# Kernel optimization log

Measured on AMD Instinct MI355X. Metric: run time of the kernel, lower is better.

## Reference

```python
import jax, jax.numpy as jnp
import numpy as np

B, S, D = 4, 1024, 1024      # batch, seq, dim
H = 1024                     # moe_inter_dim
E = 16                       # n_routed_experts
K = 2                        # n_activated_experts (top-k)
N_IN = 2                     # experts that consume x instead of embeddings
NSH = 2                      # n_shared_experts


def setup_inputs() -> dict:
    key = jax.random.key(0)
    ks = jax.random.split(key, 10)
    s = 0.02
    return {
        "embeddings": jax.random.normal(ks[0], (B, S, D), dtype=jnp.float32),
        "x": jax.random.normal(ks[1], (B * S, D), dtype=jnp.float32),
        "gate_w": jax.random.normal(ks[2], (E, D), dtype=jnp.float32) * s,
        "W1": jax.random.normal(ks[3], (E, D, H), dtype=jnp.float32) * s,
        "B1": jnp.zeros((E, H), dtype=jnp.float32),
        "W2": jax.random.normal(ks[4], (E, H, D), dtype=jnp.float32) * s,
        "B2": jnp.zeros((E, D), dtype=jnp.float32),
        "W3": jax.random.normal(ks[5], (E, D, H), dtype=jnp.float32) * s,
        "B3": jnp.zeros((E, H), dtype=jnp.float32),
        "sW1": jax.random.normal(ks[6], (D, NSH * H), dtype=jnp.float32) * s,
        "sB1": jnp.zeros((NSH * H,), dtype=jnp.float32),
        "sW2": jax.random.normal(ks[7], (NSH * H, D), dtype=jnp.float32) * s,
        "sB2": jnp.zeros((D,), dtype=jnp.float32),
    }


def _experts(inp, W1, B1, W2, B2, W3, B3):
    # SwiGLU expert applied for a stack of experts: inp [T,D], W* [e,...]
    h = jax.nn.silu(jnp.einsum('td,edh->eth', inp, W1) + B1[:, None, :]) \
        * (jnp.einsum('td,edh->eth', inp, W3) + B3[:, None, :])
    return jnp.einsum('eth,ehd->etd', h, W2) + B2[:, None, :]


def reference(embeddings, x, gate_w, W1, B1, W2, B2, W3, B3, sW1, sB1, sW2, sB2):
    shape = embeddings.shape
    emb = embeddings.reshape(-1, D)                       # [T, D]
    # Gate: softmax scores in fp32; n_groups==1, bias is None -> no group masking
    scores = jax.nn.softmax((emb @ gate_w.T).astype(jnp.float32), axis=-1)  # [T, E]
    top_w, top_i = jax.lax.top_k(scores, K)               # weights == gathered original_scores
    weights = top_w.astype(emb.dtype)                     # route_scale = 1.0
    # Combine coefficient per (token, expert): sum of routing weights of slots hitting e
    c = jnp.einsum('tk,tke->te', weights,
                   jax.nn.one_hot(top_i, E, dtype=weights.dtype))  # [T, E]
    # First N_IN experts consume x; the rest consume the embeddings
    out_in = _experts(x, W1[:N_IN], B1[:N_IN], W2[:N_IN], B2[:N_IN], W3[:N_IN], B3[:N_IN])
    out_emb = _experts(emb, W1[N_IN:], B1[N_IN:], W2[N_IN:], B2[N_IN:], W3[N_IN:], B3[N_IN:])
    y = jnp.einsum('te,etd->td', c, jnp.concatenate([out_in, out_emb], axis=0))
    # Shared experts (applied to every token)
    z = jax.nn.silu(emb @ sW1 + sB1) @ sW2 + sB2
    return (y + z).reshape(shape)
```

## Files before the change

### kernel.cpp

```cpp
#include <hip/hip_runtime.h>

#define T_TOK 4096
#define DIM   1024
#define HID   1024
#define NEXP  16
#define HSH   2048
#define NIN   2
#define MT_MAX 80

typedef __attribute__((ext_vector_type(8))) short bf8_t;
typedef __attribute__((ext_vector_type(4))) float f4_t;

__device__ __forceinline__ ushort f2b(float f) {
  unsigned u = __float_as_uint(f);
  u = (u + 0x7FFFu + ((u >> 16) & 1u)) >> 16;
  return (ushort)u;
}

__device__ __forceinline__ int tp_off(int r, int c) {
  return r * 64 + ((((c >> 3) ^ (r & 7)) << 3) | (c & 7));
}
__device__ __forceinline__ size_t tp_idx(int row, int col, int KT) {
  return ((size_t)((row >> 7) * KT + (col >> 6)) << 13) + tp_off(row & 127, col & 63);
}

__device__ __forceinline__ void gl_lds16(const ushort* g, ushort* l) {
  __builtin_amdgcn_global_load_lds(
      (const __attribute__((address_space(1))) void*)g,
      (__attribute__((address_space(3))) void*)l, 16, 0, 0);
}

__device__ __forceinline__ int src_off(int sr, int rd, int cp, int h) {
  const int cg = h * 4 + (cp ^ ((rd >> 1) & 3));
  return sr * 64 + ((cg ^ (sr & 7)) << 3);
}

template<bool DUAL>
__device__ __forceinline__ void mfma_tp(
    const ushort* pA00, const ushort* pA01,
    const ushort* pA10, const ushort* pA11,
    const ushort* b1T, const ushort* b3T,
    int oB00, int oB01, int oB10, int oB11,
    int nkt, ushort* As, ushort* Bs1, ushort* Bs3,
    f4_t acc1[4][4], f4_t acc3[4][4], int tid)
{
  const int lane = tid & 63, w = tid >> 6;
  const int wm = w & 1, wn = w >> 1;
  const int quad = lane >> 4, lr = lane & 15;
  const int dst0 = w * 1024 + lane * 8;

  auto stage = [&](int koff, ushort* dA, ushort* dB1, ushort* dB3,
                   const ushort* a0, const ushort* a1, int ob0, int ob1) {
    gl_lds16(a0 + koff, dA + dst0);
    gl_lds16(a1 + koff, dA + dst0 + 512);
    gl_lds16(b1T + ob0 + koff, dB1 + dst0);
    gl_lds16(b1T + ob1 + koff, dB1 + dst0 + 512);
    if (DUAL) {
      gl_lds16(b3T + ob0 + koff, dB3 + dst0);
      gl_lds16(b3T + ob1 + koff, dB3 + dst0 + 512);
    }
  };
  auto compute = [&](const ushort* A, const ushort* B1, const ushort* B3) {
    bf8_t af[4];
    #pragma unroll
    for (int mi = 0; mi < 4; mi++) {
      const int r = wm * 64 + mi * 16 + lr;
      af[mi] = *(const bf8_t*)&A[r * 32 + ((quad ^ ((r >> 1) & 3)) << 3)];
    }
    #pragma unroll
    for (int ni = 0; ni < 4; ni++) {
      const int n = wn * 64 + ni * 16 + lr;
      const bf8_t b1 = *(const bf8_t*)&B1[n * 32 + ((quad ^ ((n >> 1) & 3)) << 3)];
      #pragma unroll
      for (int mi = 0; mi < 4; mi++)
        acc1[mi][ni] = __builtin_amdgcn_mfma_f32_16x16x32_bf16(af[mi], b1, acc1[mi][ni], 0, 0, 0);
      if (DUAL) {
        const bf8_t b3 = *(const bf8_t*)&B3[n * 32 + ((quad ^ ((n >> 1) & 3)) << 3)];
        #pragma unroll
        for (int mi = 0; mi < 4; mi++)
          acc3[mi][ni] = __builtin_amdgcn_mfma_f32_16x16x32_bf16(af[mi], b3, acc3[mi][ni], 0, 0, 0);
      }
    }
  };

  stage(0, As, Bs1, Bs3, pA00, pA10, oB00, oB10);
  __syncthreads();
  for (int kt = 0; kt < nkt; kt++) {
    const int ko = kt << 13;
    stage(ko, As + 4096, Bs1 + 4096, Bs3 + 4096, pA01, pA11, oB01, oB11);
    compute(As, Bs1, Bs3);
    __syncthreads();
    if (kt + 1 < nkt)
      stage(ko + 8192, As, Bs1, Bs3, pA00, pA10, oB00, oB10);
    compute(As + 4096, Bs1 + 4096, Bs3 + 4096);
    __syncthreads();
  }
}

__device__ __forceinline__ void tr_chunk(const float* __restrict__ src,
                                         ushort* __restrict__ dst,
                                         int R, int C, int band, int c, int tid,
                                         ushort* ts)
{
  const int KT = R >> 6;
  const int k0 = band * 64;
  #pragma unroll
  for (int i = 0; i < 16; i++) {
    const int idx = i * 256 + tid;
    const int r = idx >> 6, c4 = idx & 63;
    const float4 v = *(const float4*)(src + (size_t)(k0 + r) * C + c * 256 + c4 * 4);
    ushort4 u;
    u.x = f2b(v.x); u.y = f2b(v.y); u.z = f2b(v.z); u.w = f2b(v.w);
    *(ushort4*)&ts[r * 256 + ((c4 ^ ((r >> 3) & 7)) << 2)] = u;
  }
  __syncthreads();
  #pragma unroll
  for (int s = 0; s < 8; s++) {
    const int idx = s * 256 + tid;
    const int n = idx >> 3, kc = idx & 7;
    ushort o[8];
    #pragma unroll
    for (int j = 0; j < 8; j++)
      o[j] = ts[(kc * 8 + j) * 256 + (((n >> 2) ^ kc) << 2) + (n & 3)];
    *(uint4*)&dst[tp_idx(c * 256 + n, k0 + kc * 8, KT)] = *(uint4*)o;
  }
}

#define PREP_BLOCKS 4864
__launch_bounds__(256, 5)
__global__ void prep(const float* __restrict__ emb, const float* __restrict__ x_,
                     const float* __restrict__ gw,
                     const float* __restrict__ W1, const float* __restrict__ W3,
                     const float* __restrict__ W2,
                     const float* __restrict__ sW1, const float* __restrict__ sW2,
                     ushort* __restrict__ etp, ushort* __restrict__ xtp,
                     ushort* __restrict__ w1tp, ushort* __restrict__ w3tp,
                     ushort* __restrict__ w2tp,
                     ushort* __restrict__ sw1tp, ushort* __restrict__ sw2tp,
                     int* __restrict__ eA, int* __restrict__ eB,
                     float* __restrict__ wA, float* __restrict__ wB)
{
  __shared__ ushort ts[64 * 256];
  const int b = blockIdx.x;
  const int t = threadIdx.x;

  if (b < 3328) {
    const float* src; ushort* dst; int R, C, band, chunk;
    if (b < 3072) {
      const int z = b >> 6, rem = b & 63;
      band = rem >> 2; chunk = rem & 3;
      const int e = z & 15;
      src = ((z < 16) ? W1 : (z < 32) ? W3 : W2) + ((size_t)e << 20);
      dst = ((z < 16) ? w1tp : (z < 32) ? w3tp : w2tp) + ((size_t)e << 20);
      R = 1024; C = 1024;
    } else if (b < 3200) {
      const int i = b - 3072; band = i >> 3; chunk = i & 7;
      src = sW1; dst = sw1tp; R = 1024; C = 2048;
    } else {
      const int i = b - 3200; band = i >> 2; chunk = i & 3;
      src = sW2; dst = sw2tp; R = 2048; C = 1024;
    }
    tr_chunk(src, dst, R, C, band, chunk, t, ts);
  } else if (b < 4352) {
    const int w = t >> 6, lane = t & 63;
    const int tok = (b - 3328) * 4 + w;
    const float* er = emb + (size_t)tok * DIM + lane * 4;
    const float4 a0 = *(const float4*)(er);
    const float4 a1 = *(const float4*)(er + 256);
    const float4 a2 = *(const float4*)(er + 512);
    const float4 a3 = *(const float4*)(er + 768);
    float pe[NEXP];
    #pragma unroll
    for (int e = 0; e < NEXP; e++) {
      const float* gr = gw + (size_t)e * DIM + lane * 4;
      const float4 g0 = *(const float4*)(gr);
      const float4 g1 = *(const float4*)(gr + 256);
      const float4 g2 = *(const float4*)(gr + 512);
      const float4 g3 = *(const float4*)(gr + 768);
      float p = a0.x * g0.x + a0.y * g0.y + a0.z * g0.z + a0.w * g0.w;
      p += a1.x * g1.x + a1.y * g1.y + a1.z * g1.z + a1.w * g1.w;
      p += a2.x * g2.x + a2.y * g2.y + a2.z * g2.z + a2.w * g2.w;
      p += a3.x * g3.x + a3.y * g3.y + a3.z * g3.z + a3.w * g3.w;
      pe[e] = p;
    }
    #pragma unroll
    for (int e = 0; e < NEXP; e++) {
      float v = pe[e];
      v += __shfl_xor(v, 1);  v += __shfl_xor(v, 2);
      v += __shfl_xor(v, 4);  v += __shfl_xor(v, 8);
      v += __shfl_xor(v, 16); v += __shfl_xor(v, 32);
      pe[e] = v;
    }
    if (lane == 0) {
      float m1 = pe[0];
      #pragma unroll
      for (int j = 1; j < NEXP; j++) m1 = fmaxf(m1, pe[j]);
      float sum = 0.f;
      #pragma unroll
      for (int j = 0; j < NEXP; j++) sum += __expf(pe[j] - m1);
      int i0 = 0; float b0 = pe[0];
      #pragma unroll
      for (int j = 1; j < NEXP; j++) if (pe[j] > b0) { b0 = pe[j]; i0 = j; }
      int i1 = -1; float b1 = -3.402823466e38f;
      #pragma unroll
      for (int j = 0; j < NEXP; j++) if (j != i0 && pe[j] > b1) { b1 = pe[j]; i1 = j; }
      const float inv = 1.0f / sum;
      eA[tok] = i0; wA[tok] = __expf(b0 - m1) * inv;
      eB[tok] = i1; wB[tok] = __expf(b1 - m1) * inv;
    }
  } else {
    const int NC = (T_TOK * DIM) / 8;
    const int c0 = (b - 4352) * 256 + t;
    for (int c = c0; c < 2 * NC; c += 512 * 256) {
      const bool isE = c < NC;
      const int g = (isE ? c : c - NC) << 3;
      const float* src = isE ? emb : x_;
      const float4 v0 = *(const float4*)(src + g);
      const float4 v1 = *(const float4*)(src + g + 4);
      ushort tt[8];
      tt[0] = f2b(v0.x); tt[1] = f2b(v0.y); tt[2] = f2b(v0.z); tt[3] = f2b(v0.w);
      tt[4] = f2b(v1.x); tt[5] = f2b(v1.y); tt[6] = f2b(v1.z); tt[7] = f2b(v1.w);
      const int row = g >> 10, col = g & 1023;
      ushort* dst = isE ? etp : xtp;
      *(uint4*)&dst[tp_idx(row, col, 16)] = *(uint4*)tt;
    }
  }
}

__global__ void build_lists(const int* __restrict__ eA, const int* __restrict__ eB,
                            const float* __restrict__ wA, const float* __restrict__ wB,
                            int* __restrict__ cnt, int* __restrict__ list,
                            float* __restrict__ wl)
{
  const int e = blockIdx.x;
  __shared__ int wsum[4];
  __shared__ int sbase;
  const int tid = threadIdx.x;
  const int lane = tid & 63, wv = tid >> 6;
  if (tid == 0) sbase = 0;
  __syncthreads();
  for (int r = 0; r < 16; r++) {
    const int tk = r * 256 + tid;
    const int a = eA[tk], bb = eB[tk];
    const bool m = (a == e) || (bb == e);
    const float w = (a == e) ? wA[tk] : wB[tk];
    const unsigned long long bal = __ballot(m);
    const int pw = __popcll(bal & ((1ULL << lane) - 1ULL));
    if (lane == 63) wsum[wv] = pw + (m ? 1 : 0);
    __syncthreads();
    int base = sbase;
    for (int k = 0; k < wv; k++) base += wsum[k];
    if (m) {
      const int pos = base + pw;
      list[e * T_TOK + pos] = tk;
      wl[e * T_TOK + pos] = w;
    }
    __syncthreads();
    if (tid == 0) sbase += wsum[0] + wsum[1] + wsum[2] + wsum[3];
    __syncthreads();
  }
  if (tid == 0) cnt[e] = sbase;
}

__global__ void scan_offs(const int* __restrict__ cnt, int* __restrict__ offp,
                          int* __restrict__ tbl)
{
  if (blockIdx.x == 0 && threadIdx.x == 0) {
    int a = 0, nm = 0;
    for (int e = 0; e < NEXP; e++) {
      offp[e] = a;
      const int c = (cnt[e] + 127) & ~127;
      for (int r = 0; r < c; r += 128) { tbl[2 * nm] = e; tbl[2 * nm + 1] = a + r; nm++; }
      a += c;
    }
    offp[NEXP] = a;
    offp[NEXP + 1] = nm;
  }
}

__launch_bounds__(256, 3)
__global__ void stage1(const ushort* __restrict__ etp, const ushort* __restrict__ xtp,
                       const ushort* __restrict__ w1tp, const ushort* __restrict__ w3tp,
                       const ushort* __restrict__ sw1tp,
                       const float* __restrict__ B1, const float* __restrict__ B3,
                       const float* __restrict__ sB1,
                       const int* __restrict__ cnt, const int* __restrict__ offp,
                       const int* __restrict__ tbl, const int* __restrict__ list,
                       ushort* __restrict__ h_tp, ushort* __restrict__ hs_tp)
{
  __shared__ ushort As[8192], Bs1[8192], Bs3[8192];
  const int tid = threadIdx.x;
  const int lane = tid & 63, w = tid >> 6;
  const int wm = w & 1, wn = w >> 1;
  const int quad = lane >> 4, lr = lane & 15;
  const int r0 = w * 32 + (lane >> 2), r1 = r0 + 16, cp = lane & 3;
  const int b = blockIdx.x;

  f4_t acc1[4][4], acc3[4][4];
  const f4_t fz = {0.f, 0.f, 0.f, 0.f};
  #pragma unroll
  for (int i = 0; i < 4; i++)
    #pragma unroll
    for (int j = 0; j < 4; j++) { acc1[i][j] = fz; acc3[i][j] = fz; }

  const int o00 = src_off(r0, r0, cp, 0), o01 = src_off(r0, r0, cp, 1);
  const int o10 = src_off(r1, r1, cp, 0), o11 = src_off(r1, r1, cp, 1);

  if (b < 512) {
    const int m0 = (b >> 4) << 7;
    const int n0 = (b & 15) << 7;
    const ushort* aT = etp + ((size_t)((m0 >> 7) * 16) << 13);
    const ushort* bT = sw1tp + ((size_t)((n0 >> 7) * 16) << 13);
    mfma_tp<false>(aT + o00, aT + o01, aT + o10, aT + o11,
                   bT, nullptr, o00, o01, o10, o11,
                   16, As, Bs1, Bs3, acc1, acc3, tid);
    #pragma unroll
    for (int mi = 0; mi < 4; mi++) {
      #pragma unroll
      for (int r = 0; r < 4; r++) {
        const int row = m0 + wm * 64 + mi * 16 + quad * 4 + r;
        #pragma unroll
        for (int ni = 0; ni < 4; ni++) {
          const int col = n0 + wn * 64 + ni * 16 + lr;
          const float v = acc1[mi][ni][r] + sB1[col];
          const float sg = 1.0f / (1.0f + __expf(-v));
          hs_tp[tp_idx(row, col, 32)] = f2b(v * sg);
        }
      }
    }
  } else {
    const int t = b - 512;
    const int mt = t >> 3;
    if (mt >= offp[NEXP + 1]) return;
    const int n0 = (t & 7) << 7;
    const int e = tbl[2 * mt], row0 = tbl[2 * mt + 1];
    const int ce = cnt[e];
    const int s0 = row0 - offp[e];
    const ushort* src = (e < NIN) ? xtp : etp;
    int sa = s0 + r0; if (sa >= ce) sa = ce - 1;
    int sb = s0 + r1; if (sb >= ce) sb = ce - 1;
    const int tokA = list[e * T_TOK + sa];
    const int tokB = list[e * T_TOK + sb];
    const ushort* tA = src + ((size_t)((tokA >> 7) * 16) << 13);
    const ushort* tB = src + ((size_t)((tokB >> 7) * 16) << 13);
    const int ra = tokA & 127, rb = tokB & 127;
    const ushort* b1T = w1tp + ((size_t)e << 20) + ((size_t)((n0 >> 7) * 16) << 13);
    const ushort* b3T = w3tp + ((size_t)e << 20) + ((size_t)((n0 >> 7) * 16) << 13);
    mfma_tp<true>(tA + src_off(ra, r0, cp, 0), tA + src_off(ra, r0, cp, 1),
                  tB + src_off(rb, r1, cp, 0), tB + src_off(rb, r1, cp, 1),
                  b1T, b3T, o00, o01, o10, o11,
                  16, As, Bs1, Bs3, acc1, acc3, tid);
    #pragma unroll
    for (int mi = 0; mi < 4; mi++) {
      #pragma unroll
      for (int r = 0; r < 4; r++) {
        const int grow = row0 + wm * 64 + mi * 16 + quad * 4 + r;
        #pragma unroll
        for (int ni = 0; ni < 4; ni++) {
          const int col = n0 + wn * 64 + ni * 16 + lr;
          const float v1 = acc1[mi][ni][r] + B1[e * HID + col];
          const float v3 = acc3[mi][ni][r] + B3[e * HID + col];
          const float sg = 1.0f / (1.0f + __expf(-v1));
          h_tp[tp_idx(grow, col, 16)] = f2b(v1 * sg * v3);
        }
      }
    }
  }
}

__launch_bounds__(256, 4)
__global__ void stage2(const ushort* __restrict__ h_tp, const ushort* __restrict__ hs_tp,
                       const ushort* __restrict__ w2tp, const ushort* __restrict__ sw2tp,
                       const float* __restrict__ B2, const float* __restrict__ sB2,
                       const int* __restrict__ cnt, const int* __restrict__ offp,
                       const int* __restrict__ tbl, const int* __restrict__ list,
                       const float* __restrict__ wl, float* __restrict__ y)
{
  __shared__ ushort As[8192], Bs[8192];
  const int tid = threadIdx.x;
  const int lane = tid & 63, w = tid >> 6;
  const int wm = w & 1, wn = w >> 1;
  const int quad = lane >> 4, lr = lane & 15;
  const int r0 = w * 32 + (lane >> 2), r1 = r0 + 16, cp = lane & 3;
  const int b = blockIdx.x;

  f4_t acc[4][4];
  const f4_t fz = {0.f, 0.f, 0.f, 0.f};
  #pragma unroll
  for (int i = 0; i < 4; i++)
    #pragma unroll
    for (int j = 0; j < 4; j++) acc[i][j] = fz;

  const int o00 = src_off(r0, r0, cp, 0), o01 = src_off(r0, r0, cp, 1);
  const int o10 = src_off(r1, r1, cp, 0), o11 = src_off(r1, r1, cp, 1);

  if (b < 256) {
    const int m0 = (b >> 3) << 7;
    const int n0 = (b & 7) << 7;
    const ushort* aT = hs_tp + ((size_t)((m0 >> 7) * 32) << 13);
    const ushort* bT = sw2tp + ((size_t)((n0 >> 7) * 32) << 13);
    mfma_tp<false>(aT + o00, aT + o01, aT + o10, aT + o11,
                   bT, nullptr, o00, o01, o10, o11,
                   32, As, Bs, Bs, acc, acc, tid);
    #pragma unroll
    for (int mi = 0; mi < 4; mi++) {
      #pragma unroll
      for (int r = 0; r < 4; r++) {
        const int row = m0 + wm * 64 + mi * 16 + quad * 4 + r;
        float* yr = y + (size_t)row * DIM;
        #pragma unroll
        for (int ni = 0; ni < 4; ni++) {
          const int col = n0 + wn * 64 + ni * 16 + lr;
          atomicAdd(&yr[col], acc[mi][ni][r] + sB2[col]);
        }
      }
    }
  } else {
    const int t = b - 256;
    const int mt = t >> 3;
    if (mt >= offp[NEXP + 1]) return;
    const int n0 = (t & 7) << 7;
    const int e = tbl[2 * mt], row0 = tbl[2 * mt + 1];
    const int ce = cnt[e];
    const int s0 = row0 - offp[e];
    const ushort* aT = h_tp + ((size_t)((row0 >> 7) * 16) << 13);
    const ushort* bT = w2tp + ((size_t)e << 20) + ((size_t)((n0 >> 7) * 16) << 13);
    mfma_tp<false>(aT + o00, aT + o01, aT + o10, aT + o11,
                   bT, nullptr, o00, o01, o10, o11,
                   16, As, Bs, Bs, acc, acc, tid);
    #pragma unroll
    for (int mi = 0; mi < 4; mi++) {
      #pragma unroll
      for (int r = 0; r < 4; r++) {
        const int rowl = s0 + wm * 64 + mi * 16 + quad * 4 + r;
        if (rowl < ce) {
          const int tok = list[e * T_TOK + rowl];
          const float wgt = wl[e * T_TOK + rowl];
          float* yr = y + (size_t)tok * DIM;
          #pragma unroll
          for (int ni = 0; ni < 4; ni++) {
            const int col = n0 + wn * 64 + ni * 16 + lr;
            atomicAdd(&yr[col], wgt * (acc[mi][ni][r] + B2[e * DIM + col]));
          }
        }
      }
    }
  }
}

extern "C" void kernel_launch(void* const* d_in, const int* in_sizes, int n_in,
                              void* d_out, int out_size, void* d_ws, size_t ws_size,
                              hipStream_t stream)
{
  const float* emb = (const float*)d_in[0];
  const float* x   = (const float*)d_in[1];
  const float* gw  = (const float*)d_in[2];
  const float* W1  = (const float*)d_in[3];
  const float* B1  = (const float*)d_in[4];
  const float* W2  = (const float*)d_in[5];
  const float* B2  = (const float*)d_in[6];
  const float* W3  = (const float*)d_in[7];
  const float* B3  = (const float*)d_in[8];
  const float* sW1 = (const float*)d_in[9];
  const float* sB1 = (const float*)d_in[10];
  const float* sW2 = (const float*)d_in[11];
  const float* sB2 = (const float*)d_in[12];
  float* y = (float*)d_out;

  char* ws = (char*)d_ws;
  const size_t MB = 1024ULL * 1024ULL;
  ushort* xtp   = (ushort*)(ws + 0);
  ushort* etp   = (ushort*)(ws + 16 * MB);
  ushort* w1tp  = (ushort*)(ws + 24 * MB);
  ushort* w3tp  = (ushort*)(ws + 56 * MB);
  ushort* w2tp  = (ushort*)(ws + 88 * MB);
  ushort* sw1tp = (ushort*)(ws + 120 * MB);
  ushort* sw2tp = (ushort*)(ws + 124 * MB);
  ushort* h_tp  = (ushort*)(ws + 148 * MB);
  ushort* hs_tp = (ushort*)(ws + 168 * MB);
  int*   cnt    = (int*)(ws + 184 * MB);
  int*   offp   = cnt + 16;
  int*   tbl    = offp + 18;
  int*   list   = (int*)(ws + 184 * MB + 1024);
  float* wl     = (float*)(ws + 184 * MB + 1024 + 262144);
  int*   eA     = (int*)(ws + 185 * MB);
  int*   eB     = eA + T_TOK;
  float* wA     = (float*)(eB + T_TOK);
  float* wB     = wA + T_TOK;

  hipMemsetAsync(y, 0, (size_t)T_TOK * DIM * sizeof(float), stream);
  prep<<<PREP_BLOCKS, 256, 0, stream>>>(emb, x, gw, W1, W3, W2, sW1, sW2,
                                        etp, xtp, w1tp, w3tp, w2tp,
                                        sw1tp, sw2tp, eA, eB, wA, wB);
  build_lists<<<NEXP, 256, 0, stream>>>(eA, eB, wA, wB, cnt, list, wl);
  scan_offs<<<1, 64, 0, stream>>>(cnt, offp, tbl);
  stage1<<<512 + MT_MAX * 8, 256, 0, stream>>>(etp, xtp, w1tp, w3tp, sw1tp,
                                               B1, B3, sB1, cnt, offp, tbl, list,
                                               h_tp, hs_tp);
  stage2<<<256 + MT_MAX * 8, 256, 0, stream>>>(h_tp, hs_tp, w2tp, sw2tp, B2, sB2,
                                               cnt, offp, tbl, list, wl, y);
}
```

Before: 524.0 us.

## Retile bf16 operand layout to 128x32 tiles for contiguous LDS staging

Changes the pre-transformed bf16 tile format from 128x64 tiles to 128x32 tiles whose swizzle matches the LDS fragment layout directly. Each K-phase can then be staged with a flat contiguous global_load_lds copy instead of per-lane swizzled source offsets, which simplifies the double-buffered loop to one stage and one compute per phase. It also pads the transpose scratch buffer in prep to reduce LDS bank conflicts, at the cost of lowering prep's occupancy hint. The trade-off is more loop iterations and barriers per GEMM, since each phase covers half the K depth it did before.

```diff
diff --git a/kernel.cpp b/kernel.cpp
--- a/kernel.cpp
+++ b/kernel.cpp
@@ -18,10 +18,15 @@
 }
 
 __device__ __forceinline__ int tp_off(int r, int c) {
-  return r * 64 + ((((c >> 3) ^ (r & 7)) << 3) | (c & 7));
+  const int R2 = r >> 1;
+  return (R2 << 6) + ((((((c >> 3) ^ R2) & 3)) | ((r & 1) << 2)) << 3) + (c & 7);
 }
 __device__ __forceinline__ size_t tp_idx(int row, int col, int KT) {
-  return ((size_t)((row >> 7) * KT + (col >> 6)) << 13) + tp_off(row & 127, col & 63);
+  return ((size_t)((row >> 7) * KT + (col >> 5)) << 12) + tp_off(row & 127, col & 31);
+}
+__device__ __forceinline__ int srcA(int sr, int cl) {
+  const int S2 = sr >> 1;
+  return (S2 << 6) + (((((cl ^ S2) & 3)) | ((sr & 1) << 2)) << 3);
 }
 
 __device__ __forceinline__ void gl_lds16(const ushort* g, ushort* l) {
@@ -30,34 +35,26 @@
       (__attribute__((address_space(3))) void*)l, 16, 0, 0);
 }
 
-__device__ __forceinline__ int src_off(int sr, int rd, int cp, int h) {
-  const int cg = h * 4 + (cp ^ ((rd >> 1) & 3));
-  return sr * 64 + ((cg ^ (sr & 7)) << 3);
-}
-
 template<bool DUAL>
 __device__ __forceinline__ void mfma_tp(
-    const ushort* pA00, const ushort* pA01,
-    const ushort* pA10, const ushort* pA11,
-    const ushort* b1T, const ushort* b3T,
-    int oB00, int oB01, int oB10, int oB11,
-    int nkt, ushort* As, ushort* Bs1, ushort* Bs3,
+    const ushort* pA0, const ushort* pA1,
+    const ushort* pB1, const ushort* pB3,
+    int nph, ushort* As, ushort* Bs1, ushort* Bs3,
     f4_t acc1[4][4], f4_t acc3[4][4], int tid)
 {
   const int lane = tid & 63, w = tid >> 6;
   const int wm = w & 1, wn = w >> 1;
   const int quad = lane >> 4, lr = lane & 15;
-  const int dst0 = w * 1024 + lane * 8;
-
-  auto stage = [&](int koff, ushort* dA, ushort* dB1, ushort* dB3,
-                   const ushort* a0, const ushort* a1, int ob0, int ob1) {
-    gl_lds16(a0 + koff, dA + dst0);
-    gl_lds16(a1 + koff, dA + dst0 + 512);
-    gl_lds16(b1T + ob0 + koff, dB1 + dst0);
-    gl_lds16(b1T + ob1 + koff, dB1 + dst0 + 512);
+  const int d0 = w * 1024 + lane * 8;
+
+  auto stage = [&](int po, ushort* dA, ushort* dB1, ushort* dB3) {
+    gl_lds16(pA0 + po, dA + d0);
+    gl_lds16(pA1 + po, dA + d0 + 512);
+    gl_lds16(pB1 + po, dB1 + d0);
+    gl_lds16(pB1 + po + 512, dB1 + d0 + 512);
     if (DUAL) {
-      gl_lds16(b3T + ob0 + koff, dB3 + dst0);
-      gl_lds16(b3T + ob1 + koff, dB3 + dst0 + 512);
+      gl_lds16(pB3 + po, dB3 + d0);
+      gl_lds16(pB3 + po + 512, dB3 + d0 + 512);
     }
   };
   auto compute = [&](const ushort* A, const ushort* B1, const ushort* B3) {
@@ -65,17 +62,20 @@
     #pragma unroll
     for (int mi = 0; mi < 4; mi++) {
       const int r = wm * 64 + mi * 16 + lr;
-      af[mi] = *(const bf8_t*)&A[r * 32 + ((quad ^ ((r >> 1) & 3)) << 3)];
+      const int R2 = r >> 1;
+      af[mi] = *(const bf8_t*)&A[(R2 << 6) + ((((quad ^ R2) & 3) | ((r & 1) << 2)) << 3)];
     }
     #pragma unroll
     for (int ni = 0; ni < 4; ni++) {
       const int n = wn * 64 + ni * 16 + lr;
-      const bf8_t b1 = *(const bf8_t*)&B1[n * 32 + ((quad ^ ((n >> 1) & 3)) << 3)];
+      const int N2 = n >> 1;
+      const int bo = (N2 << 6) + ((((quad ^ N2) & 3) | ((n & 1) << 2)) << 3);
+      const bf8_t b1 = *(const bf8_t*)&B1[bo];
       #pragma unroll
       for (int mi = 0; mi < 4; mi++)
         acc1[mi][ni] = __builtin_amdgcn_mfma_f32_16x16x32_bf16(af[mi], b1, acc1[mi][ni], 0, 0, 0);
       if (DUAL) {
-        const bf8_t b3 = *(const bf8_t*)&B3[n * 32 + ((quad ^ ((n >> 1) & 3)) << 3)];
+        const bf8_t b3 = *(const bf8_t*)&B3[bo];
         #pragma unroll
         for (int mi = 0; mi < 4; mi++)
           acc3[mi][ni] = __builtin_amdgcn_mfma_f32_16x16x32_bf16(af[mi], b3, acc3[mi][ni], 0, 0, 0);
@@ -83,16 +83,14 @@
     }
   };
 
-  stage(0, As, Bs1, Bs3, pA00, pA10, oB00, oB10);
+  stage(0, As, Bs1, Bs3);
   __syncthreads();
-  for (int kt = 0; kt < nkt; kt++) {
-    const int ko = kt << 13;
-    stage(ko, As + 4096, Bs1 + 4096, Bs3 + 4096, pA01, pA11, oB01, oB11);
-    compute(As, Bs1, Bs3);
-    __syncthreads();
-    if (kt + 1 < nkt)
-      stage(ko + 8192, As, Bs1, Bs3, pA00, pA10, oB00, oB10);
-    compute(As + 4096, Bs1 + 4096, Bs3 + 4096);
+  for (int ph = 0; ph < nph; ph++) {
+    const int cur = (ph & 1) << 12;
+    const int nxt = cur ^ 4096;
+    if (ph + 1 < nph)
+      stage((ph + 1) << 12, As + nxt, Bs1 + nxt, Bs3 + nxt);
+    compute(As + cur, Bs1 + cur, Bs3 + cur);
     __syncthreads();
   }
 }
@@ -102,7 +100,7 @@
                                          int R, int C, int band, int c, int tid,
                                          ushort* ts)
 {
-  const int KT = R >> 6;
+  const int KT = R >> 5;
   const int k0 = band * 64;
   #pragma unroll
   for (int i = 0; i < 16; i++) {
@@ -111,7 +109,7 @@
     const float4 v = *(const float4*)(src + (size_t)(k0 + r) * C + c * 256 + c4 * 4);
     ushort4 u;
     u.x = f2b(v.x); u.y = f2b(v.y); u.z = f2b(v.z); u.w = f2b(v.w);
-    *(ushort4*)&ts[r * 256 + ((c4 ^ ((r >> 3) & 7)) << 2)] = u;
+    *(ushort4*)&ts[r * 264 + ((c4 ^ ((r >> 3) & 7)) << 2)] = u;
   }
   __syncthreads();
   #pragma unroll
@@ -121,13 +119,13 @@
     ushort o[8];
     #pragma unroll
     for (int j = 0; j < 8; j++)
-      o[j] = ts[(kc * 8 + j) * 256 + (((n >> 2) ^ kc) << 2) + (n & 3)];
+      o[j] = ts[(kc * 8 + j) * 264 + (((n >> 2) ^ kc) << 2) + (n & 3)];
     *(uint4*)&dst[tp_idx(c * 256 + n, k0 + kc * 8, KT)] = *(uint4*)o;
   }
 }
 
 #define PREP_BLOCKS 4864
-__launch_bounds__(256, 5)
+__launch_bounds__(256, 4)
 __global__ void prep(const float* __restrict__ emb, const float* __restrict__ x_,
                      const float* __restrict__ gw,
                      const float* __restrict__ W1, const float* __restrict__ W3,
@@ -140,7 +138,7 @@
                      int* __restrict__ eA, int* __restrict__ eB,
                      float* __restrict__ wA, float* __restrict__ wB)
 {
-  __shared__ ushort ts[64 * 256];
+  __shared__ ushort ts[64 * 264];
   const int b = blockIdx.x;
   const int t = threadIdx.x;
 
@@ -222,7 +220,7 @@
       tt[4] = f2b(v1.x); tt[5] = f2b(v1.y); tt[6] = f2b(v1.z); tt[7] = f2b(v1.w);
       const int row = g >> 10, col = g & 1023;
       ushort* dst = isE ? etp : xtp;
-      *(uint4*)&dst[tp_idx(row, col, 16)] = *(uint4*)tt;
+      *(uint4*)&dst[tp_idx(row, col, 32)] = *(uint4*)tt;
     }
   }
 }
@@ -293,7 +291,9 @@
   const int lane = tid & 63, w = tid >> 6;
   const int wm = w & 1, wn = w >> 1;
   const int quad = lane >> 4, lr = lane & 15;
-  const int r0 = w * 32 + (lane >> 2), r1 = r0 + 16, cp = lane & 3;
+  const int rd0 = w * 32 + (lane >> 2), rd1 = rd0 + 16;
+  const int cl = (lane & 3) ^ ((lane >> 3) & 3);
+  const int dl = w * 1024 + lane * 8;
   const int b = blockIdx.x;
 
   f4_t acc1[4][4], acc3[4][4];
@@ -303,17 +303,13 @@
     #pragma unroll
     for (int j = 0; j < 4; j++) { acc1[i][j] = fz; acc3[i][j] = fz; }
 
-  const int o00 = src_off(r0, r0, cp, 0), o01 = src_off(r0, r0, cp, 1);
-  const int o10 = src_off(r1, r1, cp, 0), o11 = src_off(r1, r1, cp, 1);
-
   if (b < 512) {
     const int m0 = (b >> 4) << 7;
     const int n0 = (b & 15) << 7;
-    const ushort* aT = etp + ((size_t)((m0 >> 7) * 16) << 13);
-    const ushort* bT = sw1tp + ((size_t)((n0 >> 7) * 16) << 13);
-    mfma_tp<false>(aT + o00, aT + o01, aT + o10, aT + o11,
-                   bT, nullptr, o00, o01, o10, o11,
-                   16, As, Bs1, Bs3, acc1, acc3, tid);
+    const ushort* aT = etp + (((size_t)(m0 >> 7) * 32) << 12);
+    const ushort* bT = sw1tp + (((size_t)(n0 >> 7) * 32) << 12);
+    mfma_tp<false>(aT + dl, aT + dl + 512, bT + dl, nullptr,
+                   32, As, Bs1, Bs3, acc1, acc3, tid);
     #pragma unroll
     for (int mi = 0; mi < 4; mi++) {
       #pragma unroll
@@ -324,7 +320,7 @@
           const int col = n0 + wn * 64 + ni * 16 + lr;
           const float v = acc1[mi][ni][r] + sB1[col];
           const float sg = 1.0f / (1.0f + __expf(-v));
-          hs_tp[tp_idx(row, col, 32)] = f2b(v * sg);
+          hs_tp[tp_idx(row, col, 64)] = f2b(v * sg);
         }
       }
     }
@@ -337,19 +333,16 @@
     const int ce = cnt[e];
     const int s0 = row0 - offp[e];
     const ushort* src = (e < NIN) ? xtp : etp;
-    int sa = s0 + r0; if (sa >= ce) sa = ce - 1;
-    int sb = s0 + r1; if (sb >= ce) sb = ce - 1;
+    int sa = s0 + rd0; if (sa >= ce) sa = ce - 1;
+    int sb = s0 + rd1; if (sb >= ce) sb = ce - 1;
     const int tokA = list[e * T_TOK + sa];
     const int tokB = list[e * T_TOK + sb];
-    const ushort* tA = src + ((size_t)((tokA >> 7) * 16) << 13);
-    const ushort* tB = src + ((size_t)((tokB >> 7) * 16) << 13);
-    const int ra = tokA & 127, rb = tokB & 127;
-    const ushort* b1T = w1tp + ((size_t)e << 20) + ((size_t)((n0 >> 7) * 16) << 13);
-    const ushort* b3T = w3tp + ((size_t)e << 20) + ((size_t)((n0 >> 7) * 16) << 13);
-    mfma_tp<true>(tA + src_off(ra, r0, cp, 0), tA + src_off(ra, r0, cp, 1),
-                  tB + src_off(rb, r1, cp, 0), tB + src_off(rb, r1, cp, 1),
-                  b1T, b3T, o00, o01, o10, o11,
-                  16, As, Bs1, Bs3, acc1, acc3, tid);
+    const ushort* pA0 = src + (((size_t)(tokA >> 7) * 32) << 12) + srcA(tokA & 127, cl);
+    const ushort* pA1 = src + (((size_t)(tokB >> 7) * 32) << 12) + srcA(tokB & 127, cl);
+    const ushort* b1T = w1tp + ((size_t)e << 20) + (((size_t)(n0 >> 7) * 32) << 12);
+    const ushort* b3T = w3tp + ((size_t)e << 20) + (((size_t)(n0 >> 7) * 32) << 12);
+    mfma_tp<true>(pA0, pA1, b1T + dl, b3T + dl,
+                  32, As, Bs1, Bs3, acc1, acc3, tid);
     #pragma unroll
     for (int mi = 0; mi < 4; mi++) {
       #pragma unroll
@@ -361,7 +354,7 @@
           const float v1 = acc1[mi][ni][r] + B1[e * HID + col];
           const float v3 = acc3[mi][ni][r] + B3[e * HID + col];
           const float sg = 1.0f / (1.0f + __expf(-v1));
-          h_tp[tp_idx(grow, col, 16)] = f2b(v1 * sg * v3);
+          h_tp[tp_idx(grow, col, 32)] = f2b(v1 * sg * v3);
         }
       }
     }
@@ -381,7 +374,7 @@
   const int lane = tid & 63, w = tid >> 6;
   const int wm = w & 1, wn = w >> 1;
   const int quad = lane >> 4, lr = lane & 15;
-  const int r0 = w * 32 + (lane >> 2), r1 = r0 + 16, cp = lane & 3;
+  const int dl = w * 1024 + lane * 8;
   const int b = blockIdx.x;
 
   f4_t acc[4][4];
@@ -391,17 +384,13 @@
     #pragma unroll
     for (int j = 0; j < 4; j++) acc[i][j] = fz;
 
-  const int o00 = src_off(r0, r0, cp, 0), o01 = src_off(r0, r0, cp, 1);
-  const int o10 = src_off(r1, r1, cp, 0), o11 = src_off(r1, r1, cp, 1);
-
   if (b < 256) {
     const int m0 = (b >> 3) << 7;
     const int n0 = (b & 7) << 7;
-    const ushort* aT = hs_tp + ((size_t)((m0 >> 7) * 32) << 13);
-    const ushort* bT = sw2tp + ((size_t)((n0 >> 7) * 32) << 13);
-    mfma_tp<false>(aT + o00, aT + o01, aT + o10, aT + o11,
-                   bT, nullptr, o00, o01, o10, o11,
-                   32, As, Bs, Bs, acc, acc, tid);
+    const ushort* aT = hs_tp + (((size_t)(m0 >> 7) * 64) << 12);
+    const ushort* bT = sw2tp + (((size_t)(n0 >> 7) * 64) << 12);
+    mfma_tp<false>(aT + dl, aT + dl + 512, bT + dl, nullptr,
+                   64, As, Bs, Bs, acc, acc, tid);
     #pragma unroll
     for (int mi = 0; mi < 4; mi++) {
       #pragma unroll
@@ -423,11 +412,10 @@
     const int e = tbl[2 * mt], row0 = tbl[2 * mt + 1];
     const int ce = cnt[e];
     const int s0 = row0 - offp[e];
-    const ushort* aT = h_tp + ((size_t)((row0 >> 7) * 16) << 13);
-    const ushort* bT = w2tp + ((size_t)e << 20) + ((size_t)((n0 >> 7) * 16) << 13);
-    mfma_tp<false>(aT + o00, aT + o01, aT + o10, aT + o11,
-                   bT, nullptr, o00, o01, o10, o11,
-                   16, As, Bs, Bs, acc, acc, tid);
+    const ushort* aT = h_tp + (((size_t)(row0 >> 7) * 32) << 12);
+    const ushort* bT = w2tp + ((size_t)e << 20) + (((size_t)(n0 >> 7) * 32) << 12);
+    mfma_tp<false>(aT + dl, aT + dl + 512, bT + dl, nullptr,
+                   32, As, Bs, Bs, acc, acc, tid);
     #pragma unroll
     for (int mi = 0; mi < 4; mi++) {
       #pragma unroll
```

After: 475.0 us. 9.4% less time.
